# Kernel optimization log

Measured on AMD Instinct MI355X. Metric: run time of the kernel, lower is better.

The kernel has to match this reference:

```python
import jax, jax.numpy as jnp
import numpy as np

B, I, H = 8192, 1024, 1024

def setup_inputs() -> dict:
    key = jax.random.key(0)
    ks = jax.random.split(key, 5)
    return {
        "x": jax.random.normal(ks[0], (B, I), dtype=jnp.float32),
        "m_prev": jax.random.normal(ks[1], (B, H), dtype=jnp.float32),
        "c_prev": jax.random.normal(ks[2], (B, H), dtype=jnp.float32),
        "w_m": jax.random.normal(ks[3], (H, 8 * H), dtype=jnp.float32),
        "w_inputs": jax.random.normal(ks[4], (I, 8 * H), dtype=jnp.float32),
    }

def reference(x, m_prev, c_prev, w_m, w_inputs):
    hidden = w_m.shape[0]
    m_mat = m_prev @ w_m              # [B, 8H]
    in_mat = x @ w_inputs             # [B, 8H]
    # 8-way split along feature dim
    ms = jnp.split(m_mat, 8, axis=1)
    xs = jnp.split(in_mat, 8, axis=1)
    sig, th, rl = jax.nn.sigmoid, jnp.tanh, jax.nn.relu
    l1_0 = sig(xs[0] + ms[0])
    l1_1 = rl(xs[1] + ms[1])
    l1_2 = sig(xs[2] + ms[2])
    l1_3 = rl(xs[3] * ms[3])
    l1_4 = th(xs[4] + ms[4])
    l1_5 = sig(xs[5] + ms[5])
    l1_6 = th(xs[6] + ms[6])
    l1_7 = sig(xs[7] + ms[7])
    l2_0 = th(l1_0 * l1_1)
    l2_1 = th(l1_2 + l1_3)
    l2_2 = th(l1_4 * l1_5)
    l2_3 = sig(l1_6 + l1_7)
    l2_0 = th(l2_0 + c_prev)
    new_c = l2_0 * l2_1
    l3_1 = th(l2_2 + l2_3)
    new_m = th(new_c * l3_1)
    return (new_m, new_c)
```

## Files before the change

kernel.cpp:

```cpp
#include <hip/hip_runtime.h>
#include <stdint.h>
#include <stddef.h>


typedef _Float16 half8 __attribute__((ext_vector_type(8)));
typedef float f32x4 __attribute__((ext_vector_type(4)));
typedef float float4v __attribute__((ext_vector_type(4)));

__device__ __forceinline__ float fsig(float x) { return 1.0f / (1.0f + __expf(-x)); }
__device__ __forceinline__ float ftanh(float x) { return 2.0f * fsig(2.0f * x) - 1.0f; }
__device__ __forceinline__ unsigned int packh(_Float16 a, _Float16 b) {
  union { unsigned int u; _Float16 h[2]; } p;
  p.h[0] = a; p.h[1] = b; return p.u;
}

__global__ __launch_bounds__(256, 2) void nascell_main(
    const float* __restrict__ x,
    const float* __restrict__ m_prev,
    const float* __restrict__ c_prev,
    const float* __restrict__ w_inputs,
    const float* __restrict__ w_m,
    float* __restrict__ out) {
  __shared__ short lds[17408];
  const int tid = threadIdx.x;
  const int wid = tid >> 6;
  const int lane = tid & 63;
  const int row0 = blockIdx.y * 256;
  const int h0 = blockIdx.x * 16;
  const int m16 = lane & 15;
  const int q = lane >> 4;

  const int bmat = tid >> 7;
  const int bg = (tid >> 4) & 7;
  const int bkp = (tid & 15) * 2;
  const float* wsrc = bmat ? w_m : w_inputs;
  const float* wrow_base = wsrc + (size_t)bkp * 8192 + (size_t)bg * 1024 + (size_t)h0;
  short* bh = lds + bmat * 4352 + bg * 544 + (bkp ^ ((bg & 3) << 3));
  short* bl = bh + 8704;

  const float* axp[4];
  const float* amp[4];
#pragma unroll
  for (int r = 0; r < 4; ++r) {
    const size_t arow = (size_t)(row0 + wid * 64 + r * 16 + m16);
    axp[r] = x + arow * 1024 + q * 8;
    amp[r] = m_prev + arow * 1024 + q * 8;
  }

  f32x4 acc[4][9];
#pragma unroll
  for (int r = 0; r < 4; ++r)
#pragma unroll
    for (int gg = 0; gg < 9; ++gg) acc[r][gg] = (f32x4)0.0f;

  for (int kt = 0; kt < 32; ++kt) {
    const float* wr = wrow_base + (size_t)kt * 32 * 8192;
    float4v b0 = *(const float4v*)(wr);
    float4v b1 = *(const float4v*)(wr + 4);
    float4v b2 = *(const float4v*)(wr + 8);
    float4v b3 = *(const float4v*)(wr + 12);
    float4v d0 = *(const float4v*)(wr + 8192);
    float4v d1 = *(const float4v*)(wr + 8196);
    float4v d2 = *(const float4v*)(wr + 8200);
    float4v d3 = *(const float4v*)(wr + 8204);

    float4v xa[4][2];
#pragma unroll
    for (int r = 0; r < 4; ++r) {
      xa[r][0] = *(const float4v*)(axp[r] + kt * 32);
      xa[r][1] = *(const float4v*)(axp[r] + kt * 32 + 4);
    }

    __syncthreads();

#pragma unroll
    for (int n = 0; n < 16; ++n) {
      const float r0 = (n < 4 ? b0[n & 3] : n < 8 ? b1[n & 3] : n < 12 ? b2[n & 3] : b3[n & 3]);
      const float r1 = (n < 4 ? d0[n & 3] : n < 8 ? d1[n & 3] : n < 12 ? d2[n & 3] : d3[n & 3]);
      const _Float16 h0v = (_Float16)r0;
      const _Float16 h1v = (_Float16)r1;
      *(unsigned int*)(bh + n * 32) = packh(h0v, h1v);
      const _Float16 l0v = (_Float16)(r0 - (float)h0v);
      const _Float16 l1v = (_Float16)(r1 - (float)h1v);
      *(unsigned int*)(bl + n * 32) = packh(l0v, l1v);
    }

    half8 axh[4], axl[4];
#pragma unroll
    for (int r = 0; r < 4; ++r)
#pragma unroll
      for (int j = 0; j < 8; ++j) {
        const float v = xa[r][j >> 2][j & 3];
        const _Float16 hv = (_Float16)v;
        axh[r][j] = hv;
        axl[r][j] = (_Float16)(v - (float)hv);
      }

    __syncthreads();

    float4v ma[4][2];
#pragma unroll
    for (int r = 0; r < 4; ++r) {
      ma[r][0] = *(const float4v*)(amp[r] + kt * 32);
      ma[r][1] = *(const float4v*)(amp[r] + kt * 32 + 4);
    }

#pragma unroll
    for (int c = 0; c < 8; ++c) {
      const int qs = (q ^ (c & 3)) * 8;
      const int bo = c * 544 + m16 * 32 + qs;
      half8 bxh = *(const half8*)(lds + bo);
      half8 bxl = *(const half8*)(lds + 8704 + bo);
#pragma unroll
      for (int r = 0; r < 4; ++r) {
        f32x4 t = acc[r][c];
        t = __builtin_amdgcn_mfma_f32_16x16x32_f16(axh[r], bxh, t, 0, 0, 0);
        t = __builtin_amdgcn_mfma_f32_16x16x32_f16(axh[r], bxl, t, 0, 0, 0);
        t = __builtin_amdgcn_mfma_f32_16x16x32_f16(axl[r], bxh, t, 0, 0, 0);
        acc[r][c] = t;
      }
    }

    half8 amh[4], aml[4];
#pragma unroll
    for (int r = 0; r < 4; ++r)
#pragma unroll
      for (int j = 0; j < 8; ++j) {
        const float v = ma[r][j >> 2][j & 3];
        const _Float16 hv = (_Float16)v;
        amh[r][j] = hv;
        aml[r][j] = (_Float16)(v - (float)hv);
      }

#pragma unroll
    for (int c = 0; c < 8; ++c) {
      const int qs = (q ^ (c & 3)) * 8;
      const int bo = 4352 + c * 544 + m16 * 32 + qs;
      half8 bmh = *(const half8*)(lds + bo);
      half8 bml = *(const half8*)(lds + 8704 + bo);
      const int tgt = (c == 3) ? 8 : c;
#pragma unroll
      for (int r = 0; r < 4; ++r) {
        f32x4 t = acc[r][tgt];
        t = __builtin_amdgcn_mfma_f32_16x16x32_f16(amh[r], bmh, t, 0, 0, 0);
        t = __builtin_amdgcn_mfma_f32_16x16x32_f16(amh[r], bml, t, 0, 0, 0);
        t = __builtin_amdgcn_mfma_f32_16x16x32_f16(aml[r], bmh, t, 0, 0, 0);
        acc[r][tgt] = t;
      }
    }
  }

  float* out_m = out;
  float* out_c = out + (size_t)8192 * 1024;
  const int h = h0 + m16;
#pragma unroll
  for (int r = 0; r < 4; ++r) {
#pragma unroll
    for (int i = 0; i < 4; ++i) {
      const int grow = row0 + wid * 64 + r * 16 + q * 4 + i;
      const float p0 = acc[r][0][i], p1 = acc[r][1][i], p2 = acc[r][2][i];
      const float x3 = acc[r][3][i], p4 = acc[r][4][i], p5 = acc[r][5][i];
      const float p6 = acc[r][6][i], p7 = acc[r][7][i], m3 = acc[r][8][i];
      const float cp = c_prev[(size_t)grow * 1024 + h];
      float l1_0 = fsig(p0);
      float l1_1 = fmaxf(p1, 0.0f);
      float l1_2 = fsig(p2);
      float l1_3 = fmaxf(x3 * m3, 0.0f);
      float l1_4 = ftanh(p4);
      float l1_5 = fsig(p5);
      float l1_6 = ftanh(p6);
      float l1_7 = fsig(p7);
      float l2_0 = ftanh(l1_0 * l1_1);
      float l2_1 = ftanh(l1_2 + l1_3);
      float l2_2 = ftanh(l1_4 * l1_5);
      float l2_3 = fsig(l1_6 + l1_7);
      float l2_0b = ftanh(l2_0 + cp);
      float nc = l2_0b * l2_1;
      float l3_1 = ftanh(l2_2 + l2_3);
      float nm = ftanh(nc * l3_1);
      out_m[(size_t)grow * 1024 + h] = nm;
      out_c[(size_t)grow * 1024 + h] = nc;
    }
  }
}

extern "C" void kernel_launch(void* const* d_in, const int* in_sizes, int n_in,
                              void* d_out, int out_size, void* d_ws, size_t ws_size,
                              hipStream_t stream) {
  (void)in_sizes; (void)n_in; (void)out_size; (void)d_ws; (void)ws_size;
  const float* x        = (const float*)d_in[0];
  const float* m_prev   = (const float*)d_in[1];
  const float* c_prev   = (const float*)d_in[2];
  const float* w_m      = (const float*)d_in[3];
  const float* w_inputs = (const float*)d_in[4];
  float* out = (float*)d_out;

  dim3 grid(64, 32);
  nascell_main<<<grid, 256, 0, stream>>>(x, m_prev, c_prev, w_inputs, w_m, out);
}
```

Baseline: 1.028 ms.

## Pre-split operands to fp16 hi/lo in workspace and double-buffer B via async LDS loads

Adds preprocessing kernels that convert the weights into a pre-swizzled fp16 hi/lo tiled layout and split x and m_prev into fp16 hi/lo arrays in the workspace. The main GEMM kernel then loads B tiles directly into LDS with global_load_lds, double-buffered so the next tile prefetches while the current one feeds the MFMAs, which removes per-iteration conversion work and one barrier. This costs extra launches and roughly 128MB of workspace traffic, and the old kernel is kept as a fallback when the workspace is too small.

```diff
diff --git a/kernel.cpp b/kernel.cpp
--- a/kernel.cpp
+++ b/kernel.cpp
@@ -6,46 +6,97 @@
 typedef _Float16 half8 __attribute__((ext_vector_type(8)));
 typedef float f32x4 __attribute__((ext_vector_type(4)));
 typedef float float4v __attribute__((ext_vector_type(4)));
+typedef unsigned int u32;
+typedef u32 u32x4 __attribute__((ext_vector_type(4)));
 
 __device__ __forceinline__ float fsig(float x) { return 1.0f / (1.0f + __expf(-x)); }
 __device__ __forceinline__ float ftanh(float x) { return 2.0f * fsig(2.0f * x) - 1.0f; }
-__device__ __forceinline__ unsigned int packh(_Float16 a, _Float16 b) {
-  union { unsigned int u; _Float16 h[2]; } p;
+__device__ __forceinline__ u32 packh(_Float16 a, _Float16 b) {
+  union { u32 u; _Float16 h[2]; } p;
   p.h[0] = a; p.h[1] = b; return p.u;
 }
 
-__global__ __launch_bounds__(256, 2) void nascell_main(
-    const float* __restrict__ x,
-    const float* __restrict__ m_prev,
+__device__ __forceinline__ void gload16(const void* g, void* l) {
+  __builtin_amdgcn_global_load_lds(
+      (const __attribute__((address_space(1))) void*)g,
+      (__attribute__((address_space(3))) void*)l, 16, 0, 0);
+}
+
+__global__ __launch_bounds__(256) void prep_b(
+    const float* __restrict__ w_inputs, const float* __restrict__ w_m,
+    u32* __restrict__ wsB) {
+  const int kt = blockIdx.x;
+  const int hblk = blockIdx.y;
+  const int tid = threadIdx.x;
+  const int n = tid & 15;
+  const int g = (tid >> 4) & 7;
+  const int mat = tid >> 7;
+  const float* w = mat ? w_m : w_inputs;
+  const float* src = w + (size_t)kt * 32 * 8192 + (size_t)g * 1024 + hblk * 16 + n;
+  const int kx4 = ((n >> 1) & 3) << 2;
+  u32 hw[16], lw[16];
+#pragma unroll
+  for (int k2 = 0; k2 < 16; ++k2) {
+    const float v0 = src[(size_t)(2 * k2) * 8192];
+    const float v1 = src[(size_t)(2 * k2 + 1) * 8192];
+    const _Float16 h0 = (_Float16)v0, h1 = (_Float16)v1;
+    hw[k2 ^ kx4] = packh(h0, h1);
+    lw[k2 ^ kx4] = packh((_Float16)(v0 - (float)h0), (_Float16)(v1 - (float)h1));
+  }
+  u32* dhi = wsB + ((size_t)kt * 64 + hblk) * 8192 + mat * 2048 + g * 256 + n * 16;
+  u32* dlo = dhi + 4096;
+#pragma unroll
+  for (int t4 = 0; t4 < 4; ++t4) {
+    u32x4 a = {hw[t4 * 4], hw[t4 * 4 + 1], hw[t4 * 4 + 2], hw[t4 * 4 + 3]};
+    *(u32x4*)(dhi + t4 * 4) = a;
+    u32x4 b = {lw[t4 * 4], lw[t4 * 4 + 1], lw[t4 * 4 + 2], lw[t4 * 4 + 3]};
+    *(u32x4*)(dlo + t4 * 4) = b;
+  }
+}
+
+__global__ __launch_bounds__(256) void split_a(
+    const float4v* __restrict__ in, half8* __restrict__ hi, half8* __restrict__ lo) {
+  const size_t idx = (size_t)blockIdx.x * 256 + threadIdx.x;
+  const float4v a = in[idx * 2];
+  const float4v b = in[idx * 2 + 1];
+  half8 h, l;
+#pragma unroll
+  for (int j = 0; j < 4; ++j) {
+    const float v = a[j]; const _Float16 hv = (_Float16)v;
+    h[j] = hv; l[j] = (_Float16)(v - (float)hv);
+  }
+#pragma unroll
+  for (int j = 0; j < 4; ++j) {
+    const float v = b[j]; const _Float16 hv = (_Float16)v;
+    h[4 + j] = hv; l[4 + j] = (_Float16)(v - (float)hv);
+  }
+  hi[idx] = h; lo[idx] = l;
+}
+
+__global__ __launch_bounds__(256, 2) void nascell_fast(
+    const _Float16* __restrict__ xh_g, const _Float16* __restrict__ xl_g,
+    const _Float16* __restrict__ mh_g, const _Float16* __restrict__ ml_g,
+    const u32* __restrict__ wsB,
     const float* __restrict__ c_prev,
-    const float* __restrict__ w_inputs,
-    const float* __restrict__ w_m,
     float* __restrict__ out) {
-  __shared__ short lds[17408];
+  __shared__ short lds[32768];
   const int tid = threadIdx.x;
   const int wid = tid >> 6;
   const int lane = tid & 63;
   const int row0 = blockIdx.y * 256;
-  const int h0 = blockIdx.x * 16;
+  const int hblk = blockIdx.x;
   const int m16 = lane & 15;
   const int q = lane >> 4;
-
-  const int bmat = tid >> 7;
-  const int bg = (tid >> 4) & 7;
-  const int bkp = (tid & 15) * 2;
-  const float* wsrc = bmat ? w_m : w_inputs;
-  const float* wrow_base = wsrc + (size_t)bkp * 8192 + (size_t)bg * 1024 + (size_t)h0;
-  short* bh = lds + bmat * 4352 + bg * 544 + (bkp ^ ((bg & 3) << 3));
-  short* bl = bh + 8704;
-
-  const float* axp[4];
-  const float* amp[4];
-#pragma unroll
-  for (int r = 0; r < 4; ++r) {
-    const size_t arow = (size_t)(row0 + wid * 64 + r * 16 + m16);
-    axp[r] = x + arow * 1024 + q * 8;
-    amp[r] = m_prev + arow * 1024 + q * 8;
-  }
+  const int qsw = (q ^ ((m16 >> 1) & 3)) * 8;
+
+  const size_t arow = (size_t)(row0 + wid * 64 + m16);
+  const _Float16* xhb = xh_g + arow * 1024 + q * 8;
+  const _Float16* xlb = xl_g + arow * 1024 + q * 8;
+  const _Float16* mhb = mh_g + arow * 1024 + q * 8;
+  const _Float16* mlb = ml_g + arow * 1024 + q * 8;
+
+  const char* wsb = (const char*)wsB + (size_t)hblk * 32768 + wid * 8192 + lane * 16;
+  char* ldsb0 = (char*)lds + wid * 8192;
 
   f32x4 acc[4][9];
 #pragma unroll
@@ -53,64 +104,36 @@
 #pragma unroll
     for (int gg = 0; gg < 9; ++gg) acc[r][gg] = (f32x4)0.0f;
 
+#pragma unroll
+  for (int i = 0; i < 8; ++i) gload16(wsb + i * 1024, ldsb0 + i * 1024);
+
   for (int kt = 0; kt < 32; ++kt) {
-    const float* wr = wrow_base + (size_t)kt * 32 * 8192;
-    float4v b0 = *(const float4v*)(wr);
-    float4v b1 = *(const float4v*)(wr + 4);
-    float4v b2 = *(const float4v*)(wr + 8);
-    float4v b3 = *(const float4v*)(wr + 12);
-    float4v d0 = *(const float4v*)(wr + 8192);
-    float4v d1 = *(const float4v*)(wr + 8196);
-    float4v d2 = *(const float4v*)(wr + 8200);
-    float4v d3 = *(const float4v*)(wr + 8204);
-
-    float4v xa[4][2];
+    __syncthreads();
+
+    half8 axh[4], axl[4], amh[4], aml[4];
 #pragma unroll
     for (int r = 0; r < 4; ++r) {
-      xa[r][0] = *(const float4v*)(axp[r] + kt * 32);
-      xa[r][1] = *(const float4v*)(axp[r] + kt * 32 + 4);
-    }
-
-    __syncthreads();
-
-#pragma unroll
-    for (int n = 0; n < 16; ++n) {
-      const float r0 = (n < 4 ? b0[n & 3] : n < 8 ? b1[n & 3] : n < 12 ? b2[n & 3] : b3[n & 3]);
-      const float r1 = (n < 4 ? d0[n & 3] : n < 8 ? d1[n & 3] : n < 12 ? d2[n & 3] : d3[n & 3]);
-      const _Float16 h0v = (_Float16)r0;
-      const _Float16 h1v = (_Float16)r1;
-      *(unsigned int*)(bh + n * 32) = packh(h0v, h1v);
-      const _Float16 l0v = (_Float16)(r0 - (float)h0v);
-      const _Float16 l1v = (_Float16)(r1 - (float)h1v);
-      *(unsigned int*)(bl + n * 32) = packh(l0v, l1v);
-    }
-
-    half8 axh[4], axl[4];
-#pragma unroll
-    for (int r = 0; r < 4; ++r)
-#pragma unroll
-      for (int j = 0; j < 8; ++j) {
-        const float v = xa[r][j >> 2][j & 3];
-        const _Float16 hv = (_Float16)v;
-        axh[r][j] = hv;
-        axl[r][j] = (_Float16)(v - (float)hv);
-      }
-
-    __syncthreads();
-
-    float4v ma[4][2];
-#pragma unroll
-    for (int r = 0; r < 4; ++r) {
-      ma[r][0] = *(const float4v*)(amp[r] + kt * 32);
-      ma[r][1] = *(const float4v*)(amp[r] + kt * 32 + 4);
-    }
+      axh[r] = *(const half8*)(xhb + (size_t)r * 16384 + kt * 32);
+      axl[r] = *(const half8*)(xlb + (size_t)r * 16384 + kt * 32);
+      amh[r] = *(const half8*)(mhb + (size_t)r * 16384 + kt * 32);
+      aml[r] = *(const half8*)(mlb + (size_t)r * 16384 + kt * 32);
+    }
+    __builtin_amdgcn_sched_barrier(0);
+    if (kt < 31) {
+      const char* src = wsb + (size_t)(kt + 1) * 2097152;
+      char* dst = (char*)lds + ((kt + 1) & 1) * 32768 + wid * 8192;
+#pragma unroll
+      for (int i = 0; i < 8; ++i) gload16(src + i * 1024, dst + i * 1024);
+    }
+    __builtin_amdgcn_sched_barrier(0);
+
+    const short* bb = lds + (kt & 1) * 16384;
 
 #pragma unroll
     for (int c = 0; c < 8; ++c) {
-      const int qs = (q ^ (c & 3)) * 8;
-      const int bo = c * 544 + m16 * 32 + qs;
-      half8 bxh = *(const half8*)(lds + bo);
-      half8 bxl = *(const half8*)(lds + 8704 + bo);
+      const int bo = c * 512 + m16 * 32 + qsw;
+      const half8 bxh = *(const half8*)(bb + bo);
+      const half8 bxl = *(const half8*)(bb + 8192 + bo);
 #pragma unroll
       for (int r = 0; r < 4; ++r) {
         f32x4 t = acc[r][c];
@@ -121,23 +144,11 @@
       }
     }
 
-    half8 amh[4], aml[4];
-#pragma unroll
-    for (int r = 0; r < 4; ++r)
-#pragma unroll
-      for (int j = 0; j < 8; ++j) {
-        const float v = ma[r][j >> 2][j & 3];
-        const _Float16 hv = (_Float16)v;
-        amh[r][j] = hv;
-        aml[r][j] = (_Float16)(v - (float)hv);
-      }
-
 #pragma unroll
     for (int c = 0; c < 8; ++c) {
-      const int qs = (q ^ (c & 3)) * 8;
-      const int bo = 4352 + c * 544 + m16 * 32 + qs;
-      half8 bmh = *(const half8*)(lds + bo);
-      half8 bml = *(const half8*)(lds + 8704 + bo);
+      const int bo = 4096 + c * 512 + m16 * 32 + qsw;
+      const half8 bmh = *(const half8*)(bb + bo);
+      const half8 bml = *(const half8*)(bb + 8192 + bo);
       const int tgt = (c == 3) ? 8 : c;
 #pragma unroll
       for (int r = 0; r < 4; ++r) {
@@ -152,7 +163,7 @@
 
   float* out_m = out;
   float* out_c = out + (size_t)8192 * 1024;
-  const int h = h0 + m16;
+  const int h = hblk * 16 + m16;
 #pragma unroll
   for (int r = 0; r < 4; ++r) {
 #pragma unroll
@@ -184,10 +195,180 @@
   }
 }
 
+__global__ __launch_bounds__(256, 2) void nascell_main(
+    const float* __restrict__ x,
+    const float* __restrict__ m_prev,
+    const float* __restrict__ c_prev,
+    const float* __restrict__ w_inputs,
+    const float* __restrict__ w_m,
+    float* __restrict__ out) {
+  __shared__ short lds[17408];
+  const int tid = threadIdx.x;
+  const int wid = tid >> 6;
+  const int lane = tid & 63;
+  const int row0 = blockIdx.y * 256;
+  const int h0 = blockIdx.x * 16;
+  const int m16 = lane & 15;
+  const int q = lane >> 4;
+
+  const int bmat = tid >> 7;
+  const int bg = (tid >> 4) & 7;
+  const int bkp = (tid & 15) * 2;
+  const float* wsrc = bmat ? w_m : w_inputs;
+  const float* wrow_base = wsrc + (size_t)bkp * 8192 + (size_t)bg * 1024 + (size_t)h0;
+  short* bh = lds + bmat * 4352 + bg * 544 + (bkp ^ ((bg & 3) << 3));
+  short* bl = bh + 8704;
+
+  const float* axp[4];
+  const float* amp[4];
+#pragma unroll
+  for (int r = 0; r < 4; ++r) {
+    const size_t arow = (size_t)(row0 + wid * 64 + r * 16 + m16);
+    axp[r] = x + arow * 1024 + q * 8;
+    amp[r] = m_prev + arow * 1024 + q * 8;
+  }
+
+  f32x4 acc[4][9];
+#pragma unroll
+  for (int r = 0; r < 4; ++r)
+#pragma unroll
+    for (int gg = 0; gg < 9; ++gg) acc[r][gg] = (f32x4)0.0f;
+
+  for (int kt = 0; kt < 32; ++kt) {
+    const float* wr = wrow_base + (size_t)kt * 32 * 8192;
+    float4v b0 = *(const float4v*)(wr);
+    float4v b1 = *(const float4v*)(wr + 4);
+    float4v b2 = *(const float4v*)(wr + 8);
+    float4v b3 = *(const float4v*)(wr + 12);
+    float4v d0 = *(const float4v*)(wr + 8192);
+    float4v d1 = *(const float4v*)(wr + 8196);
+    float4v d2 = *(const float4v*)(wr + 8200);
+    float4v d3 = *(const float4v*)(wr + 8204);
+
+    float4v xa[4][2];
+#pragma unroll
+    for (int r = 0; r < 4; ++r) {
+      xa[r][0] = *(const float4v*)(axp[r] + kt * 32);
+      xa[r][1] = *(const float4v*)(axp[r] + kt * 32 + 4);
+    }
+
+    __syncthreads();
+
+#pragma unroll
+    for (int n = 0; n < 16; ++n) {
+      const float r0 = (n < 4 ? b0[n & 3] : n < 8 ? b1[n & 3] : n < 12 ? b2[n & 3] : b3[n & 3]);
+      const float r1 = (n < 4 ? d0[n & 3] : n < 8 ? d1[n & 3] : n < 12 ? d2[n & 3] : d3[n & 3]);
+      const _Float16 h0v = (_Float16)r0;
+      const _Float16 h1v = (_Float16)r1;
+      *(u32*)(bh + n * 32) = packh(h0v, h1v);
+      const _Float16 l0v = (_Float16)(r0 - (float)h0v);
+      const _Float16 l1v = (_Float16)(r1 - (float)h1v);
+      *(u32*)(bl + n * 32) = packh(l0v, l1v);
+    }
+
+    half8 axh[4], axl[4];
+#pragma unroll
+    for (int r = 0; r < 4; ++r)
+#pragma unroll
+      for (int j = 0; j < 8; ++j) {
+        const float v = xa[r][j >> 2][j & 3];
+        const _Float16 hv = (_Float16)v;
+        axh[r][j] = hv;
+        axl[r][j] = (_Float16)(v - (float)hv);
+      }
+
+    __syncthreads();
+
+    float4v ma[4][2];
+#pragma unroll
+    for (int r = 0; r < 4; ++r) {
+      ma[r][0] = *(const float4v*)(amp[r] + kt * 32);
+      ma[r][1] = *(const float4v*)(amp[r] + kt * 32 + 4);
+    }
+
+#pragma unroll
+    for (int c = 0; c < 8; ++c) {
+      const int qs = (q ^ (c & 3)) * 8;
+      const int bo = c * 544 + m16 * 32 + qs;
+      half8 bxh = *(const half8*)(lds + bo);
+      half8 bxl = *(const half8*)(lds + 8704 + bo);
+#pragma unroll
+      for (int r = 0; r < 4; ++r) {
+        f32x4 t = acc[r][c];
+        t = __builtin_amdgcn_mfma_f32_16x16x32_f16(axh[r], bxh, t, 0, 0, 0);
+        t = __builtin_amdgcn_mfma_f32_16x16x32_f16(axh[r], bxl, t, 0, 0, 0);
+        t = __builtin_amdgcn_mfma_f32_16x16x32_f16(axl[r], bxh, t, 0, 0, 0);
+        acc[r][c] = t;
+      }
+    }
+
+    half8 amh[4], aml[4];
+#pragma unroll
+    for (int r = 0; r < 4; ++r)
+#pragma unroll
+      for (int j = 0; j < 8; ++j) {
+        const float v = ma[r][j >> 2][j & 3];
+        const _Float16 hv = (_Float16)v;
+        amh[r][j] = hv;
+        aml[r][j] = (_Float16)(v - (float)hv);
+      }
+
+#pragma unroll
+    for (int c = 0; c < 8; ++c) {
+      const int qs = (q ^ (c & 3)) * 8;
+      const int bo = 4352 + c * 544 + m16 * 32 + qs;
+      half8 bmh = *(const half8*)(lds + bo);
+      half8 bml = *(const half8*)(lds + 8704 + bo);
+      const int tgt = (c == 3) ? 8 : c;
+#pragma unroll
+      for (int r = 0; r < 4; ++r) {
+        f32x4 t = acc[r][tgt];
+        t = __builtin_amdgcn_mfma_f32_16x16x32_f16(amh[r], bmh, t, 0, 0, 0);
+        t = __builtin_amdgcn_mfma_f32_16x16x32_f16(amh[r], bml, t, 0, 0, 0);
+        t = __builtin_amdgcn_mfma_f32_16x16x32_f16(aml[r], bmh, t, 0, 0, 0);
+        acc[r][tgt] = t;
+      }
+    }
+  }
+
+  float* out_m = out;
+  float* out_c = out + (size_t)8192 * 1024;
+  const int h = h0 + m16;
+#pragma unroll
+  for (int r = 0; r < 4; ++r) {
+#pragma unroll
+    for (int i = 0; i < 4; ++i) {
+      const int grow = row0 + wid * 64 + r * 16 + q * 4 + i;
+      const float p0 = acc[r][0][i], p1 = acc[r][1][i], p2 = acc[r][2][i];
+      const float x3 = acc[r][3][i], p4 = acc[r][4][i], p5 = acc[r][5][i];
+      const float p6 = acc[r][6][i], p7 = acc[r][7][i], m3 = acc[r][8][i];
+      const float cp = c_prev[(size_t)grow * 1024 + h];
+      float l1_0 = fsig(p0);
+      float l1_1 = fmaxf(p1, 0.0f);
+      float l1_2 = fsig(p2);
+      float l1_3 = fmaxf(x3 * m3, 0.0f);
+      float l1_4 = ftanh(p4);
+      float l1_5 = fsig(p5);
+      float l1_6 = ftanh(p6);
+      float l1_7 = fsig(p7);
+      float l2_0 = ftanh(l1_0 * l1_1);
+      float l2_1 = ftanh(l1_2 + l1_3);
+      float l2_2 = ftanh(l1_4 * l1_5);
+      float l2_3 = fsig(l1_6 + l1_7);
+      float l2_0b = ftanh(l2_0 + cp);
+      float nc = l2_0b * l2_1;
+      float l3_1 = ftanh(l2_2 + l2_3);
+      float nm = ftanh(nc * l3_1);
+      out_m[(size_t)grow * 1024 + h] = nm;
+      out_c[(size_t)grow * 1024 + h] = nc;
+    }
+  }
+}
+
 extern "C" void kernel_launch(void* const* d_in, const int* in_sizes, int n_in,
                               void* d_out, int out_size, void* d_ws, size_t ws_size,
                               hipStream_t stream) {
-  (void)in_sizes; (void)n_in; (void)out_size; (void)d_ws; (void)ws_size;
+  (void)in_sizes; (void)n_in; (void)out_size;
   const float* x        = (const float*)d_in[0];
   const float* m_prev   = (const float*)d_in[1];
   const float* c_prev   = (const float*)d_in[2];
@@ -195,6 +376,18 @@
   const float* w_inputs = (const float*)d_in[4];
   float* out = (float*)d_out;
 
-  dim3 grid(64, 32);
-  nascell_main<<<grid, 256, 0, stream>>>(x, m_prev, c_prev, w_inputs, w_m, out);
-}
+  if (ws_size >= 134217728ull && d_ws != nullptr) {
+    u32* wsB = (u32*)d_ws;
+    _Float16* xh = (_Float16*)((char*)d_ws + 67108864);
+    _Float16* xl = xh + 8388608;
+    _Float16* mh = xl + 8388608;
+    _Float16* ml = mh + 8388608;
+    prep_b<<<dim3(32, 64), 256, 0, stream>>>(w_inputs, w_m, wsB);
+    split_a<<<4096, 256, 0, stream>>>((const float4v*)x, (half8*)xh, (half8*)xl);
+    split_a<<<4096, 256, 0, stream>>>((const float4v*)m_prev, (half8*)mh, (half8*)ml);
+    nascell_fast<<<dim3(64, 32), 256, 0, stream>>>(xh, xl, mh, ml, wsB, c_prev, out);
+  } else {
+    dim3 grid(64, 32);
+    nascell_main<<<grid, 256, 0, stream>>>(x, m_prev, c_prev, w_inputs, w_m, out);
+  }
+}
```

Result: faster. 873.0 us (-15.1%).
